# Optimization experiments

Measured on AMD Instinct MI355X. Metric: run time of the kernel, lower is better.

## Reference

```python
import jax, jax.numpy as jnp
import numpy as np

EPS = 1e-7  # K.epsilon()


def setup_inputs() -> dict:
    key = jax.random.key(0)
    k1, k2 = jax.random.split(key)
    B, m, n = 4096, 256, 256
    y = jax.random.normal(k1, (B, n), dtype=jnp.float32)
    A = jax.random.normal(k2, (m, n), dtype=jnp.float32)
    b = jnp.ones((m,), dtype=jnp.float32)   # Ac = 0 < b, so c is interior
    c = jnp.zeros((n,), dtype=jnp.float32)
    return {"y": y, "A": A, "b": b, "c": c}


def reference(y, A, b, c):
    # Ac and residual b - Ac  -> [m]
    Ac = A @ c
    b_minus_Ac = b - Ac
    # A (y - c): broadcast-matmul expressed as einsum  -> [B, m]
    y_minus_c = y - c
    A_dot = jnp.einsum("mn,bn->bm", A, y_minus_c)
    # candidate intersection scalars along the line y->c
    ip = b_minus_Ac / (A_dot + EPS)
    cand = jnp.where(ip > 1.0, 2.0, ip)
    cand = jnp.where(cand < 0.0, 2.0, cand)
    alpha = jnp.min(cand, axis=-1, keepdims=True)      # [B, 1]
    alpha = jnp.where(alpha > 1.0, 1.0, alpha)          # interior point -> keep y
    z = alpha * y + (1.0 - alpha) * c
    return z
```

## Files before the change

### kernel.cpp

```cpp
#include <hip/hip_runtime.h>
#include <hip/hip_bf16.h>

#define EPS 1e-7f

typedef __attribute__((ext_vector_type(8))) short short8;
typedef __attribute__((ext_vector_type(4))) float f32x4;

__device__ __forceinline__ unsigned pk(float a, float b) {
    __hip_bfloat162 h2 = __float22bfloat162_rn(make_float2(a, b));
    unsigned r; __builtin_memcpy(&r, &h2, 4); return r;
}

__global__ __launch_bounds__(256)
void prep_kernel(const float* __restrict__ A, const float* __restrict__ bb,
                 const float* __restrict__ c, short* __restrict__ Aswz,
                 float* __restrict__ Ac, float* __restrict__ bmAc)
{
    const int blk = blockIdx.x;
    const int t = threadIdx.x;
    if (blk < 32) {
        const int u = blk * 256 + t;
        const int l = u & 63;
        const int s = (u >> 6) & 7;
        const int T = u >> 9;
        const int row = T * 16 + (l & 15);
        const int n0 = s * 32 + ((l >> 4) & 3) * 8;
        const float4* ap = (const float4*)(A + (size_t)row * 256 + n0);
        float4 f0 = ap[0];
        float4 f1 = ap[1];
        uint4 v;
        v.x = pk(f0.x, f0.y); v.y = pk(f0.z, f0.w);
        v.z = pk(f1.x, f1.y); v.w = pk(f1.z, f1.w);
        *(uint4*)(Aswz + (size_t)u * 8) = v;
    } else {
        const int g = blk - 32;
        const int w = t >> 6;
        const int lane = t & 63;
        const int row = g * 4 + w;
        const float4* a4 = (const float4*)(A + (size_t)row * 256);
        const float4* c4 = (const float4*)c;
        float4 av = a4[lane], cv = c4[lane];
        float p = av.x * cv.x + av.y * cv.y + av.z * cv.z + av.w * cv.w;
        #pragma unroll
        for (int off = 1; off < 64; off <<= 1) p += __shfl_xor(p, off);
        if (lane == 0) {
            Ac[row] = p;
            bmAc[row] = bb[row] - p;
        }
    }
}

__global__ __launch_bounds__(512)
void gemm_kernel(const float* __restrict__ y, const float* __restrict__ c,
                 const short* __restrict__ Aswz, const float* __restrict__ Ac,
                 const float* __restrict__ bmAc, float* __restrict__ z)
{
    __shared__ float red[8][16];
    __shared__ float alphas[16];

    const int t    = threadIdx.x;
    const int w    = t >> 6;
    const int lane = t & 63;
    const int lr   = lane & 15;
    const int lg   = lane >> 4;
    const int b0   = blockIdx.x * 16;

    f32x4 acc0 = {0.f, 0.f, 0.f, 0.f};
    f32x4 acc1 = {0.f, 0.f, 0.f, 0.f};

    const int yrow = b0 + lr;
    const float4* yp = (const float4*)(y + (size_t)yrow * 256) + lg * 2;

    const int MT0 = w * 2, MT1 = MT0 + 1;
    const short8* bp0 = (const short8*)Aswz + (size_t)(MT0 * 8) * 64 + lane;
    const short8* bp1 = (const short8*)Aswz + (size_t)(MT1 * 8) * 64 + lane;

    #pragma unroll
    for (int s = 0; s < 8; ++s) {
        float4 f0 = yp[8 * s];
        float4 f1 = yp[8 * s + 1];
        uint4 au;
        au.x = pk(f0.x, f0.y); au.y = pk(f0.z, f0.w);
        au.z = pk(f1.x, f1.y); au.w = pk(f1.z, f1.w);
        short8 af; __builtin_memcpy(&af, &au, 16);
        short8 bf0 = bp0[s * 64];
        short8 bf1 = bp1[s * 64];
        acc0 = __builtin_amdgcn_mfma_f32_16x16x32_bf16(af, bf0, acc0, 0, 0, 0);
        acc1 = __builtin_amdgcn_mfma_f32_16x16x32_bf16(af, bf1, acc1, 0, 0, 0);
    }

    const int m0 = MT0 * 16 + lr;
    const int m1 = MT1 * 16 + lr;
    const float Ac0 = Ac[m0], Ac1 = Ac[m1];
    const float bm0 = bmAc[m0], bm1 = bmAc[m1];

    float cmin[4];
    #pragma unroll
    for (int q = 0; q < 4; ++q) {
        float d0 = acc0[q] - Ac0;
        float d1 = acc1[q] - Ac1;
        float ip0 = bm0 / (d0 + EPS);
        float ip1 = bm1 / (d1 + EPS);
        float c0 = (ip0 > 1.f || ip0 < 0.f) ? 2.f : ip0;
        float c1 = (ip1 > 1.f || ip1 < 0.f) ? 2.f : ip1;
        cmin[q] = fminf(c0, c1);
    }
    #pragma unroll
    for (int q = 0; q < 4; ++q) {
        float v = cmin[q];
        v = fminf(v, __shfl_xor(v, 1));
        v = fminf(v, __shfl_xor(v, 2));
        v = fminf(v, __shfl_xor(v, 4));
        v = fminf(v, __shfl_xor(v, 8));
        cmin[q] = v;
    }
    if (lr == 0) {
        #pragma unroll
        for (int q = 0; q < 4; ++q) red[w][lg * 4 + q] = cmin[q];
    }
    __syncthreads();

    if (t < 16) {
        float a = red[0][t];
        #pragma unroll
        for (int i = 1; i < 8; ++i) a = fminf(a, red[i][t]);
        alphas[t] = fminf(a, 1.0f);
    }
    __syncthreads();

    const float4* y4 = (const float4*)y;
    const float4* c4 = (const float4*)c;
    float4* z4 = (float4*)z;
    #pragma unroll
    for (int k = 0; k < 2; ++k) {
        int pos = t + k * 512;
        int row = pos >> 6;
        int col = pos & 63;
        float al = alphas[row];
        float4 yv = y4[(size_t)(b0 + row) * 64 + col];
        float4 cv = c4[col];
        float4 o;
        o.x = fmaf(al, yv.x - cv.x, cv.x);
        o.y = fmaf(al, yv.y - cv.y, cv.y);
        o.z = fmaf(al, yv.z - cv.z, cv.z);
        o.w = fmaf(al, yv.w - cv.w, cv.w);
        z4[(size_t)(b0 + row) * 64 + col] = o;
    }
}

extern "C" void kernel_launch(void* const* d_in, const int* in_sizes, int n_in,
                              void* d_out, int out_size, void* d_ws, size_t ws_size,
                              hipStream_t stream) {
    const float* y = (const float*)d_in[0];
    const float* A = (const float*)d_in[1];
    const float* b = (const float*)d_in[2];
    const float* c = (const float*)d_in[3];
    float* z = (float*)d_out;

    short* Aswz = (short*)d_ws;
    float* Acp  = (float*)((char*)d_ws + 65536 * 2);
    float* bmAcp = Acp + 256;

    const int B = in_sizes[0] / 256;

    prep_kernel<<<96, 256, 0, stream>>>(A, b, c, Aswz, Acp, bmAcp);
    gemm_kernel<<<B / 16, 512, 0, stream>>>(y, c, Aswz, Acp, bmAcp, z);
}
```

Baseline: 67.47 us.

## Fuse A prep into GEMM kernel, stage y-c in LDS, compute Ac via MFMA

Drops the separate prep kernel that converted A to swizzled bf16 and computed Ac. Each GEMM block now reads fp32 A directly from global memory and converts it in registers, and it computes A·c with extra MFMAs using c as the A operand. y-c is staged once in LDS and reused for both the MFMA input and the epilogue, so y is not read twice from global memory. This removes one launch and the extra pass over y, at the cost of redundant fp32 A loads and conversions in every block and twice the MFMA work. Ac is now computed in bf16 rather than fp32.

```diff
diff --git a/kernel.cpp b/kernel.cpp
--- a/kernel.cpp
+++ b/kernel.cpp
@@ -2,6 +2,7 @@
 #include <hip/hip_bf16.h>
 
 #define EPS 1e-7f
+#define LDSW 260
 
 typedef __attribute__((ext_vector_type(8))) short short8;
 typedef __attribute__((ext_vector_type(4))) float f32x4;
@@ -11,50 +12,19 @@
     unsigned r; __builtin_memcpy(&r, &h2, 4); return r;
 }
 
-__global__ __launch_bounds__(256)
-void prep_kernel(const float* __restrict__ A, const float* __restrict__ bb,
-                 const float* __restrict__ c, short* __restrict__ Aswz,
-                 float* __restrict__ Ac, float* __restrict__ bmAc)
-{
-    const int blk = blockIdx.x;
-    const int t = threadIdx.x;
-    if (blk < 32) {
-        const int u = blk * 256 + t;
-        const int l = u & 63;
-        const int s = (u >> 6) & 7;
-        const int T = u >> 9;
-        const int row = T * 16 + (l & 15);
-        const int n0 = s * 32 + ((l >> 4) & 3) * 8;
-        const float4* ap = (const float4*)(A + (size_t)row * 256 + n0);
-        float4 f0 = ap[0];
-        float4 f1 = ap[1];
-        uint4 v;
-        v.x = pk(f0.x, f0.y); v.y = pk(f0.z, f0.w);
-        v.z = pk(f1.x, f1.y); v.w = pk(f1.z, f1.w);
-        *(uint4*)(Aswz + (size_t)u * 8) = v;
-    } else {
-        const int g = blk - 32;
-        const int w = t >> 6;
-        const int lane = t & 63;
-        const int row = g * 4 + w;
-        const float4* a4 = (const float4*)(A + (size_t)row * 256);
-        const float4* c4 = (const float4*)c;
-        float4 av = a4[lane], cv = c4[lane];
-        float p = av.x * cv.x + av.y * cv.y + av.z * cv.z + av.w * cv.w;
-        #pragma unroll
-        for (int off = 1; off < 64; off <<= 1) p += __shfl_xor(p, off);
-        if (lane == 0) {
-            Ac[row] = p;
-            bmAc[row] = bb[row] - p;
-        }
-    }
+__device__ __forceinline__ short8 mk8(float4 f0, float4 f1) {
+    uint4 u;
+    u.x = pk(f0.x, f0.y); u.y = pk(f0.z, f0.w);
+    u.z = pk(f1.x, f1.y); u.w = pk(f1.z, f1.w);
+    short8 r; __builtin_memcpy(&r, &u, 16); return r;
 }
 
-__global__ __launch_bounds__(512)
-void gemm_kernel(const float* __restrict__ y, const float* __restrict__ c,
-                 const short* __restrict__ Aswz, const float* __restrict__ Ac,
-                 const float* __restrict__ bmAc, float* __restrict__ z)
+__global__ __launch_bounds__(512, 1)
+void fused_kernel(const float* __restrict__ y, const float* __restrict__ A,
+                  const float* __restrict__ bb, const float* __restrict__ c,
+                  float* __restrict__ z)
 {
+    __shared__ float ymc[16][LDSW];
     __shared__ float red[8][16];
     __shared__ float alphas[16];
 
@@ -65,42 +35,64 @@
     const int lg   = lane >> 4;
     const int b0   = blockIdx.x * 16;
 
-    f32x4 acc0 = {0.f, 0.f, 0.f, 0.f};
-    f32x4 acc1 = {0.f, 0.f, 0.f, 0.f};
+    const float4* y4  = (const float4*)y;
+    const float4* c4g = (const float4*)c;
+    float4* z4 = (float4*)z;
 
-    const int yrow = b0 + lr;
-    const float4* yp = (const float4*)(y + (size_t)yrow * 256) + lg * 2;
+    #pragma unroll
+    for (int k = 0; k < 2; ++k) {
+        int pos = t + k * 512;
+        int row = pos >> 6, col4 = pos & 63;
+        float4 yv = y4[(size_t)(b0 + row) * 64 + col4];
+        float4 cv = c4g[col4];
+        float4 r;
+        r.x = yv.x - cv.x; r.y = yv.y - cv.y;
+        r.z = yv.z - cv.z; r.w = yv.w - cv.w;
+        *(float4*)&ymc[row][col4 * 4] = r;
+    }
+    __syncthreads();
 
-    const int MT0 = w * 2, MT1 = MT0 + 1;
-    const short8* bp0 = (const short8*)Aswz + (size_t)(MT0 * 8) * 64 + lane;
-    const short8* bp1 = (const short8*)Aswz + (size_t)(MT1 * 8) * 64 + lane;
+    f32x4 acc0  = {0.f,0.f,0.f,0.f};
+    f32x4 acc1  = {0.f,0.f,0.f,0.f};
+    f32x4 accc0 = {0.f,0.f,0.f,0.f};
+    f32x4 accc1 = {0.f,0.f,0.f,0.f};
+
+    const int MT0 = 2 * w, MT1 = MT0 + 1;
+    const float* a0 = A + (size_t)(MT0 * 16 + lr) * 256;
+    const float* a1 = A + (size_t)(MT1 * 16 + lr) * 256;
 
     #pragma unroll
     for (int s = 0; s < 8; ++s) {
-        float4 f0 = yp[8 * s];
-        float4 f1 = yp[8 * s + 1];
-        uint4 au;
-        au.x = pk(f0.x, f0.y); au.y = pk(f0.z, f0.w);
-        au.z = pk(f1.x, f1.y); au.w = pk(f1.z, f1.w);
-        short8 af; __builtin_memcpy(&af, &au, 16);
-        short8 bf0 = bp0[s * 64];
-        short8 bf1 = bp1[s * 64];
-        acc0 = __builtin_amdgcn_mfma_f32_16x16x32_bf16(af, bf0, acc0, 0, 0, 0);
-        acc1 = __builtin_amdgcn_mfma_f32_16x16x32_bf16(af, bf1, acc1, 0, 0, 0);
+        const int col = 32 * s + 8 * lg;
+        float4 yv0 = *(const float4*)&ymc[lr][col];
+        float4 yv1 = *(const float4*)&ymc[lr][col + 4];
+        short8 af = mk8(yv0, yv1);
+        float4 a00 = *(const float4*)(a0 + col);
+        float4 a01 = *(const float4*)(a0 + col + 4);
+        float4 a10 = *(const float4*)(a1 + col);
+        float4 a11 = *(const float4*)(a1 + col + 4);
+        short8 bf0 = mk8(a00, a01);
+        short8 bf1 = mk8(a10, a11);
+        float4 cv0 = *(const float4*)(c + col);
+        float4 cv1 = *(const float4*)(c + col + 4);
+        short8 cf = mk8(cv0, cv1);
+
+        acc0  = __builtin_amdgcn_mfma_f32_16x16x32_bf16(af, bf0, acc0,  0, 0, 0);
+        acc1  = __builtin_amdgcn_mfma_f32_16x16x32_bf16(af, bf1, acc1,  0, 0, 0);
+        accc0 = __builtin_amdgcn_mfma_f32_16x16x32_bf16(cf, bf0, accc0, 0, 0, 0);
+        accc1 = __builtin_amdgcn_mfma_f32_16x16x32_bf16(cf, bf1, accc1, 0, 0, 0);
     }
 
     const int m0 = MT0 * 16 + lr;
     const int m1 = MT1 * 16 + lr;
-    const float Ac0 = Ac[m0], Ac1 = Ac[m1];
-    const float bm0 = bmAc[m0], bm1 = bmAc[m1];
+    const float bm0 = bb[m0] - accc0[0];
+    const float bm1 = bb[m1] - accc1[0];
 
     float cmin[4];
     #pragma unroll
     for (int q = 0; q < 4; ++q) {
-        float d0 = acc0[q] - Ac0;
-        float d1 = acc1[q] - Ac1;
-        float ip0 = bm0 / (d0 + EPS);
-        float ip1 = bm1 / (d1 + EPS);
+        float ip0 = bm0 / (acc0[q] + EPS);
+        float ip1 = bm1 / (acc1[q] + EPS);
         float c0 = (ip0 > 1.f || ip0 < 0.f) ? 2.f : ip0;
         float c1 = (ip1 > 1.f || ip1 < 0.f) ? 2.f : ip1;
         cmin[q] = fminf(c0, c1);
@@ -128,23 +120,19 @@
     }
     __syncthreads();
 
-    const float4* y4 = (const float4*)y;
-    const float4* c4 = (const float4*)c;
-    float4* z4 = (float4*)z;
     #pragma unroll
     for (int k = 0; k < 2; ++k) {
         int pos = t + k * 512;
-        int row = pos >> 6;
-        int col = pos & 63;
+        int row = pos >> 6, col4 = pos & 63;
         float al = alphas[row];
-        float4 yv = y4[(size_t)(b0 + row) * 64 + col];
-        float4 cv = c4[col];
+        float4 m  = *(const float4*)&ymc[row][col4 * 4];
+        float4 cv = c4g[col4];
         float4 o;
-        o.x = fmaf(al, yv.x - cv.x, cv.x);
-        o.y = fmaf(al, yv.y - cv.y, cv.y);
-        o.z = fmaf(al, yv.z - cv.z, cv.z);
-        o.w = fmaf(al, yv.w - cv.w, cv.w);
-        z4[(size_t)(b0 + row) * 64 + col] = o;
+        o.x = fmaf(al, m.x, cv.x);
+        o.y = fmaf(al, m.y, cv.y);
+        o.z = fmaf(al, m.z, cv.z);
+        o.w = fmaf(al, m.w, cv.w);
+        z4[(size_t)(b0 + row) * 64 + col4] = o;
     }
 }
 
@@ -157,12 +145,6 @@
     const float* c = (const float*)d_in[3];
     float* z = (float*)d_out;
 
-    short* Aswz = (short*)d_ws;
-    float* Acp  = (float*)((char*)d_ws + 65536 * 2);
-    float* bmAcp = Acp + 256;
-
     const int B = in_sizes[0] / 256;
-
-    prep_kernel<<<96, 256, 0, stream>>>(A, b, c, Aswz, Acp, bmAcp);
-    gemm_kernel<<<B / 16, 512, 0, stream>>>(y, c, Aswz, Acp, bmAcp, z);
+    fused_kernel<<<B / 16, 512, 0, stream>>>(y, A, b, c, z);
 }
```

After: 70.40 us. 4.3% more time.
